# Optimization experiments

Measured on AMD Instinct MI355X. Metric: run time of the kernel, lower is better.

## Reference

```python
import jax, jax.numpy as jnp
import numpy as np

N, E, D, H, C = 20000, 320000, 256, 8, 32
NEG_SLOPE = 0.2


def setup_inputs() -> dict:
    key = jax.random.key(0)
    ks = jax.random.split(key, 9)
    s = 1.0 / np.sqrt(D)
    x = jax.random.normal(ks[0], (N, D), dtype=jnp.float32)
    edge_index = jax.random.randint(ks[1], (2, E), 0, N, dtype=jnp.int32)
    # positive edge weights in (0.05, 1.0] so log() is finite
    edge_attr = jax.random.uniform(ks[2], (E,), dtype=jnp.float32, minval=0.05, maxval=1.0)
    W_l = jax.random.normal(ks[3], (D, H * C), dtype=jnp.float32) * s
    b_l = jax.random.normal(ks[4], (H * C,), dtype=jnp.float32) * 0.01
    W_r = jax.random.normal(ks[5], (D, H * C), dtype=jnp.float32) * s
    b_r = jax.random.normal(ks[6], (H * C,), dtype=jnp.float32) * 0.01
    att = jax.random.normal(ks[7], (H, C), dtype=jnp.float32) * (1.0 / np.sqrt(C))
    bias = jax.random.normal(ks[8], (H * C,), dtype=jnp.float32) * 0.01
    return {"x": x, "edge_index": edge_index, "edge_attr": edge_attr,
            "W_l": W_l, "b_l": b_l, "W_r": W_r, "b_r": b_r,
            "att": att, "bias": bias}


def reference(x, edge_index, edge_attr, W_l, b_l, W_r, b_r, att, bias):
    n = x.shape[0]
    # GATv2: separate linear transforms for source (l) and target (r) nodes
    x_l = (x @ W_l + b_l).reshape(n, H, C)  # source / x_j
    x_r = (x @ W_r + b_r).reshape(n, H, C)  # target / x_i
    src, dst = edge_index[0], edge_index[1]  # flow: source_to_target, index = dst

    x_j = x_l[src]                            # [E, H, C]
    g = jax.nn.leaky_relu(x_r[dst] + x_j, NEG_SLOPE)
    alpha = jnp.einsum('ehc,hc->eh', g, att)  # [E, H]
    alpha = alpha + jnp.log(edge_attr)[:, None]

    # segment softmax over destination node (ragged edge groups)
    amax = jax.ops.segment_max(alpha, dst, num_segments=n)  # [N, H]
    ex = jnp.exp(alpha - amax[dst])
    denom = jax.ops.segment_sum(ex, dst, num_segments=n)
    alpha = ex / (denom[dst] + 1e-16)

    # message = x_j * alpha, scatter-add into destination nodes
    out = jax.ops.segment_sum(x_j * alpha[..., None], dst, num_segments=n)  # [N, H, C]
    return out.reshape(n, H * C) + bias
```

## Files before the change

kernel.cpp:

```cpp
#include <hip/hip_runtime.h>
#include <hip/hip_bf16.h>
#include <math.h>

#define DD 256
#define NHEAD 8
#define NEG_SLOPE 0.2f
#define CAP 64

typedef __attribute__((ext_vector_type(16))) float f32x16;
typedef __attribute__((ext_vector_type(8)))  short bf16x8;
typedef _Float16 h2 __attribute__((ext_vector_type(2)));

union Frag { bf16x8 v; uint4 u4; };
union HU4  { uint4 u4; h2 h[4]; };

__device__ inline uint f2bf(float f) {
    __hip_bfloat16 h = __float2bfloat16(f);
    return (uint)*(ushort*)&h;
}
__device__ inline ushort f2h(float f) {
    _Float16 h = (_Float16)f;
    return *(ushort*)&h;
}
__device__ inline h2 pkmax(h2 a, h2 b) {
    h2 d;
    asm("v_pk_max_f16 %0, %1, %2" : "=v"(d) : "v"(a), "v"(b));
    return d;
}
__device__ inline float hdot2(h2 a, h2 b, float c) {
#if __has_builtin(__builtin_amdgcn_fdot2)
    return __builtin_amdgcn_fdot2(a, b, c, false);
#else
    return c + (float)a.x * (float)b.x + (float)a.y * (float)b.y;
#endif
}

__global__ __launch_bounds__(256) void prep_kernel(const float* __restrict__ x,
                                                   const float* __restrict__ Wl,
                                                   const float* __restrict__ Wr,
                                                   ushort* __restrict__ pa,
                                                   ushort* __restrict__ pw,
                                                   int* __restrict__ counts,
                                                   int N, int Mpad) {
    int idx = blockIdx.x * 256 + threadIdx.x;
    if (idx < N) { counts[idx] = 0; return; }
    idx -= N;
    const int na = Mpad * 32;
    if (idx < na) {
        int lane = idx & 63;
        int mi   = (idx >> 6) & 1;
        int s16  = (idx >> 7) & 15;
        int tile = idx >> 11;
        int m = tile * 64 + mi * 32 + (lane & 31);
        int g = lane >> 5;
        uint4 val = {0u, 0u, 0u, 0u};
        if (m < N) {
            const float* xp = x + (size_t)m * DD + s16 * 16 + g * 4;
            float4 f0 = *(const float4*)xp;
            float4 f1 = *(const float4*)(xp + 8);
            val.x = f2bf(f0.x) | (f2bf(f0.y) << 16);
            val.y = f2bf(f0.z) | (f2bf(f0.w) << 16);
            val.z = f2bf(f1.x) | (f2bf(f1.y) << 16);
            val.w = f2bf(f1.z) | (f2bf(f1.w) << 16);
        }
        *(uint4*)(pa + (size_t)idx * 8) = val;
        return;
    }
    idx -= na;
    if (idx < 16384) {
        int lane = idx & 63;
        int s16  = (idx >> 6) & 15;
        int ng   = (idx >> 10) & 7;
        int mat  = idx >> 13;
        const float* W = mat ? Wr : Wl;
        int n  = ng * 32 + (lane & 31);
        int k0 = s16 * 16 + (lane >> 5) * 4;
        uint4 val;
        val.x = f2bf(W[(size_t)(k0 + 0) * DD + n]) | (f2bf(W[(size_t)(k0 + 1) * DD + n]) << 16);
        val.y = f2bf(W[(size_t)(k0 + 2) * DD + n]) | (f2bf(W[(size_t)(k0 + 3) * DD + n]) << 16);
        val.z = f2bf(W[(size_t)(k0 + 8) * DD + n]) | (f2bf(W[(size_t)(k0 + 9) * DD + n]) << 16);
        val.w = f2bf(W[(size_t)(k0 +10) * DD + n]) | (f2bf(W[(size_t)(k0 +11) * DD + n]) << 16);
        *(uint4*)(pw + (size_t)idx * 8) = val;
    }
}

__global__ __launch_bounds__(256) void scatter_kernel(const int* __restrict__ src,
                                                      const int* __restrict__ dst,
                                                      const float* __restrict__ w,
                                                      int* __restrict__ counts,
                                                      int2* __restrict__ csr_sw,
                                                      int E) {
    int e = blockIdx.x * 256 + threadIdx.x;
    if (e < E) {
        int d = dst[e];
        int pos = atomicAdd(&counts[d], 1);
        if (pos < CAP)
            csr_sw[((size_t)d << 6) + pos] = make_int2(src[e], __float_as_int(w[e]));
    }
}

__global__ __launch_bounds__(256, 4) void mm_kernel(const ushort* __restrict__ pa,
                                                    const ushort* __restrict__ pw,
                                                    const float* __restrict__ bl,
                                                    const float* __restrict__ br,
                                                    ushort* __restrict__ xl_h,
                                                    ushort* __restrict__ xr_h,
                                                    int N) {
    const int t    = threadIdx.x;
    const int lane = t & 63;
    const int l31  = lane & 31;
    const int g    = lane >> 5;
    const int wd   = t >> 6;
    const int tile = blockIdx.x, mat = blockIdx.y;

    const ushort* paT = pa + (size_t)tile * 2048 * 8;
    const ushort* pb  = pw + ((size_t)mat * 8192 + (size_t)(2 * wd) * 1024) * 8;

    f32x16 acc00, acc01, acc10, acc11;
    #pragma unroll
    for (int i = 0; i < 16; ++i) { acc00[i] = 0.f; acc01[i] = 0.f; acc10[i] = 0.f; acc11[i] = 0.f; }

    #pragma unroll 4
    for (int s16 = 0; s16 < 16; ++s16) {
        Frag a0, a1, b0, b1;
        a0.u4 = *(const uint4*)(paT + (size_t)((s16 * 2 + 0) * 64 + lane) * 8);
        a1.u4 = *(const uint4*)(paT + (size_t)((s16 * 2 + 1) * 64 + lane) * 8);
        b0.u4 = *(const uint4*)(pb  + (size_t)((s16     ) * 64 + lane) * 8);
        b1.u4 = *(const uint4*)(pb  + (size_t)((16 + s16) * 64 + lane) * 8);
        acc00 = __builtin_amdgcn_mfma_f32_32x32x16_bf16(a0.v, b0.v, acc00, 0, 0, 0);
        acc01 = __builtin_amdgcn_mfma_f32_32x32x16_bf16(a0.v, b1.v, acc01, 0, 0, 0);
        acc10 = __builtin_amdgcn_mfma_f32_32x32x16_bf16(a1.v, b0.v, acc10, 0, 0, 0);
        acc11 = __builtin_amdgcn_mfma_f32_32x32x16_bf16(a1.v, b1.v, acc11, 0, 0, 0);
    }

    const int n0 = wd * 64 + l31;
    const int n1 = n0 + 32;
    const float* bp = (mat == 0) ? bl : br;
    const float bv0 = bp[n0], bv1 = bp[n1];
    const int mb = tile * 64;
    ushort* dstp = (mat == 0) ? xl_h : xr_h;
    #pragma unroll
    for (int r = 0; r < 16; ++r) {
        int mloc = (r & 3) + 8 * (r >> 2) + 4 * g;
        int m0 = mb + mloc, m1 = m0 + 32;
        if (m0 < N) {
            dstp[(size_t)m0 * DD + n0] = f2h(acc00[r] + bv0);
            dstp[(size_t)m0 * DD + n1] = f2h(acc01[r] + bv1);
        }
        if (m1 < N) {
            dstp[(size_t)m1 * DD + n0] = f2h(acc10[r] + bv0);
            dstp[(size_t)m1 * DD + n1] = f2h(acc11[r] + bv1);
        }
    }
}

__global__ __launch_bounds__(256) void node_kernel(const int* __restrict__ counts,
                                                   const int2* __restrict__ csr_sw,
                                                   const ushort* __restrict__ xl_h,
                                                   const ushort* __restrict__ xr_h,
                                                   const float* __restrict__ att,
                                                   const float* __restrict__ bias,
                                                   float* __restrict__ out,
                                                   int N) {
    const int wid  = threadIdx.x >> 6;
    const int lane = threadIdx.x & 63;
    const int d = blockIdx.x * 4 + wid;
    if (d >= N) return;
    const int l31 = lane & 31;
    const int hi  = lane >> 5;
    const int c0  = l31 * 8;

    const size_t beg = (size_t)d << 6;
    const int deg = min(counts[d], CAP);

    HU4 xru; xru.u4 = *(const uint4*)(xr_h + (size_t)d * DD + c0);
    const float4 af0 = *(const float4*)(att + c0);
    const float4 af1 = *(const float4*)(att + c0 + 4);
    const h2 at0 = {(_Float16)af0.x, (_Float16)af0.y};
    const h2 at1 = {(_Float16)af0.z, (_Float16)af0.w};
    const h2 at2 = {(_Float16)af1.x, (_Float16)af1.y};
    const h2 at3 = {(_Float16)af1.z, (_Float16)af1.w};
    const h2 slope = {(_Float16)NEG_SLOPE, (_Float16)NEG_SLOPE};

    float dsum = 0.f;
    float ac[8];
    #pragma unroll
    for (int j = 0; j < 8; ++j) ac[j] = 0.f;

    auto body = [&](const HU4& xv, float we) {
        h2 a0 = xv.h[0] + xru.h[0];
        h2 a1 = xv.h[1] + xru.h[1];
        h2 a2 = xv.h[2] + xru.h[2];
        h2 a3 = xv.h[3] + xru.h[3];
        h2 g0 = pkmax(a0, a0 * slope);
        h2 g1 = pkmax(a1, a1 * slope);
        h2 g2 = pkmax(a2, a2 * slope);
        h2 g3 = pkmax(a3, a3 * slope);
        float p = hdot2(g3, at3, hdot2(g2, at2, hdot2(g1, at1, hdot2(g0, at0, 0.f))));
        p += __shfl_xor(p, 1);
        p += __shfl_xor(p, 2);
        float ev = we * __expf(p);
        dsum += ev;
        ac[0] += ev * (float)xv.h[0].x;
        ac[1] += ev * (float)xv.h[0].y;
        ac[2] += ev * (float)xv.h[1].x;
        ac[3] += ev * (float)xv.h[1].y;
        ac[4] += ev * (float)xv.h[2].x;
        ac[5] += ev * (float)xv.h[2].y;
        ac[6] += ev * (float)xv.h[3].x;
        ac[7] += ev * (float)xv.h[3].y;
    };

    const int npair = (deg + 1) >> 1;
    const int dm1   = deg - 1;
    int i = 0;
    for (; i + 2 <= npair; i += 2) {
        const int iA = 2 * i + hi;
        const int iB = iA + 2;
        int2 swA = csr_sw[beg + min(iA, dm1)];
        int2 swB = csr_sw[beg + min(iB, dm1)];
        float wA = (iA < deg) ? __int_as_float(swA.y) : 0.f;
        float wB = (iB < deg) ? __int_as_float(swB.y) : 0.f;
        HU4 xvA; xvA.u4 = *(const uint4*)(xl_h + (size_t)swA.x * DD + c0);
        HU4 xvB; xvB.u4 = *(const uint4*)(xl_h + (size_t)swB.x * DD + c0);
        body(xvA, wA);
        body(xvB, wB);
    }
    if (i < npair) {
        const int iA = 2 * i + hi;
        int2 swA = csr_sw[beg + min(iA, dm1)];
        float wA = (iA < deg) ? __int_as_float(swA.y) : 0.f;
        HU4 xvA; xvA.u4 = *(const uint4*)(xl_h + (size_t)swA.x * DD + c0);
        body(xvA, wA);
    }

    dsum += __shfl_xor(dsum, 32);
    #pragma unroll
    for (int j = 0; j < 8; ++j) ac[j] += __shfl_xor(ac[j], 32);
    const float inv = 1.f / (dsum + 1e-16f);

    const float4 bv = *(const float4*)(bias + c0 + 4 * hi);
    const int b = 4 * hi;
    float4 o;
    o.x = ac[b + 0] * inv + bv.x;
    o.y = ac[b + 1] * inv + bv.y;
    o.z = ac[b + 2] * inv + bv.z;
    o.w = ac[b + 3] * inv + bv.w;
    *(float4*)(out + (size_t)d * DD + c0 + 4 * hi) = o;
}

extern "C" void kernel_launch(void* const* d_in, const int* in_sizes, int n_in,
                              void* d_out, int out_size, void* d_ws, size_t ws_size,
                              hipStream_t stream) {
    const float* x    = (const float*)d_in[0];
    const int*   ei   = (const int*)  d_in[1];
    const float* w    = (const float*)d_in[2];
    const float* Wl   = (const float*)d_in[3];
    const float* bl   = (const float*)d_in[4];
    const float* Wr   = (const float*)d_in[5];
    const float* br   = (const float*)d_in[6];
    const float* att  = (const float*)d_in[7];
    const float* bias = (const float*)d_in[8];

    const int N = in_sizes[0] / DD;
    const int E = in_sizes[2];
    const int* src = ei;
    const int* dst = ei + E;

    const int Mtiles = (N + 63) / 64;
    const int Mpad   = Mtiles * 64;

    ushort* xr_h    = (ushort*)d_ws;
    ushort* xl_h    = xr_h + (size_t)N * DD;
    ushort* pa      = xl_h + (size_t)N * DD;
    ushort* pw      = pa + (size_t)Mpad * DD;
    int2*   csr_sw  = (int2*)(pw + 131072);
    int*    counts  = (int*)(csr_sw + (size_t)N * CAP);

    float* out = (float*)d_out;

    const int prep_total = N + Mpad * 32 + 16384;
    prep_kernel   <<<(prep_total + 255) / 256, 256, 0, stream>>>(x, Wl, Wr,
                                                                 pa, pw, counts,
                                                                 N, Mpad);
    scatter_kernel<<<(E + 255) / 256, 256, 0, stream>>>(src, dst, w, counts,
                                                        csr_sw, E);
    mm_kernel     <<<dim3(Mtiles, 2), 256, 0, stream>>>(pa, pw, bl, br,
                                                        xl_h, xr_h, N);
    node_kernel   <<<(N + 3) / 4, 256, 0, stream>>>(counts, csr_sw,
                                                    xl_h, xr_h, att, bias, out, N);
}
```

Measured before the change: 77.19 us.

## Accumulate messages in packed fp16 and unroll edge gather loop by four

```diff
diff --git a/kernel.cpp b/kernel.cpp
--- a/kernel.cpp
+++ b/kernel.cpp
@@ -183,9 +183,9 @@
     const h2 slope = {(_Float16)NEG_SLOPE, (_Float16)NEG_SLOPE};
 
     float dsum = 0.f;
-    float ac[8];
-    #pragma unroll
-    for (int j = 0; j < 8; ++j) ac[j] = 0.f;
+    h2 ac2[4];
+    #pragma unroll
+    for (int j = 0; j < 4; ++j) ac2[j] = (h2){(_Float16)0.f, (_Float16)0.f};
 
     auto body = [&](const HU4& xv, float we) {
         h2 a0 = xv.h[0] + xru.h[0];
@@ -201,32 +201,38 @@
         p += __shfl_xor(p, 2);
         float ev = we * __expf(p);
         dsum += ev;
-        ac[0] += ev * (float)xv.h[0].x;
-        ac[1] += ev * (float)xv.h[0].y;
-        ac[2] += ev * (float)xv.h[1].x;
-        ac[3] += ev * (float)xv.h[1].y;
-        ac[4] += ev * (float)xv.h[2].x;
-        ac[5] += ev * (float)xv.h[2].y;
-        ac[6] += ev * (float)xv.h[3].x;
-        ac[7] += ev * (float)xv.h[3].y;
+        _Float16 evh = (_Float16)ev;
+        h2 evv = {evh, evh};
+        ac2[0] += evv * xv.h[0];
+        ac2[1] += evv * xv.h[1];
+        ac2[2] += evv * xv.h[2];
+        ac2[3] += evv * xv.h[3];
     };
 
     const int npair = (deg + 1) >> 1;
     const int dm1   = deg - 1;
     int i = 0;
-    for (; i + 2 <= npair; i += 2) {
+    for (; i + 4 <= npair; i += 4) {
         const int iA = 2 * i + hi;
-        const int iB = iA + 2;
+        const int iB = iA + 2, iC = iA + 4, iD = iA + 6;
         int2 swA = csr_sw[beg + min(iA, dm1)];
         int2 swB = csr_sw[beg + min(iB, dm1)];
+        int2 swC = csr_sw[beg + min(iC, dm1)];
+        int2 swD = csr_sw[beg + min(iD, dm1)];
         float wA = (iA < deg) ? __int_as_float(swA.y) : 0.f;
         float wB = (iB < deg) ? __int_as_float(swB.y) : 0.f;
+        float wC = (iC < deg) ? __int_as_float(swC.y) : 0.f;
+        float wD = (iD < deg) ? __int_as_float(swD.y) : 0.f;
         HU4 xvA; xvA.u4 = *(const uint4*)(xl_h + (size_t)swA.x * DD + c0);
         HU4 xvB; xvB.u4 = *(const uint4*)(xl_h + (size_t)swB.x * DD + c0);
+        HU4 xvC; xvC.u4 = *(const uint4*)(xl_h + (size_t)swC.x * DD + c0);
+        HU4 xvD; xvD.u4 = *(const uint4*)(xl_h + (size_t)swD.x * DD + c0);
         body(xvA, wA);
         body(xvB, wB);
-    }
-    if (i < npair) {
+        body(xvC, wC);
+        body(xvD, wD);
+    }
+    for (; i < npair; ++i) {
         const int iA = 2 * i + hi;
         int2 swA = csr_sw[beg + min(iA, dm1)];
         float wA = (iA < deg) ? __int_as_float(swA.y) : 0.f;
@@ -234,6 +240,12 @@
         body(xvA, wA);
     }
 
+    float ac[8];
+    #pragma unroll
+    for (int j = 0; j < 4; ++j) {
+        ac[2 * j]     = (float)ac2[j].x;
+        ac[2 * j + 1] = (float)ac2[j].y;
+    }
     dsum += __shfl_xor(dsum, 32);
     #pragma unroll
     for (int j = 0; j < 8; ++j) ac[j] += __shfl_xor(ac[j], 32);
```

After: 74.43 us. 1.04x faster.
